# Optimization experiments

Hardware: AMD Instinct MI355X
Metric: run time of the kernel (lower is better)

## Reference

```python
import jax, jax.numpy as jnp
import numpy as np

B, N = 2, 1024
DIM, HEADS, DH, MLP = 768, 12, 64, 3072
PD = 768          # channels * patch_size^2 = 3*16*16
GRID = 16         # image_size // patch_size
DEPTH = 8
INNER = HEADS * DH


def layer_norm(x, g):
    # torch F.layer_norm with beta=0 buffer, eps=1e-5
    m = x.mean(-1, keepdims=True)
    v = ((x - m) ** 2).mean(-1, keepdims=True)
    return (x - m) / jnp.sqrt(v + 1e-5) * g


def qk_rmsnorm(x, g):
    # F.normalize(x, dim=-1) * sqrt(DH) * gamma ; gamma is [H,1,DH]
    n = jnp.linalg.norm(x, axis=-1, keepdims=True)
    return x / jnp.maximum(n, 1e-12) * (DH ** 0.5) * g


def setup_inputs() -> dict:
    key = jax.random.key(0)
    ks = jax.random.split(key, 16)
    s = 0.02
    d = {
        "patches": jax.random.normal(ks[0], (B, N, PD), dtype=jnp.float32),
        "h_idx": jax.random.randint(ks[1], (B, N), 0, GRID),
        "w_idx": jax.random.randint(ks[2], (B, N), 0, GRID),
        "image_ids": jnp.sort(jax.random.randint(ks[3], (B, N), 0, 8), axis=-1),
        "pos_h": jax.random.normal(ks[4], (GRID, PD)) * s,
        "pos_w": jax.random.normal(ks[5], (GRID, PD)) * s,
        "Wp": jax.random.normal(ks[6], (PD, DIM)) * s,
        "bp": jnp.zeros((DIM,)),
        "ln_p": jnp.ones((DIM,)),
        "ln1": jnp.ones((DEPTH, DIM)),
        "qg": jnp.ones((DEPTH, HEADS, 1, DH)),
        "kg": jnp.ones((DEPTH, HEADS, 1, DH)),
        "Wq": jax.random.normal(ks[7], (DEPTH, DIM, INNER)) * s,
        "Wkv": jax.random.normal(ks[8], (DEPTH, DIM, 2 * INNER)) * s,
        "Wo": jax.random.normal(ks[9], (DEPTH, INNER, DIM)) * s,
        "ln2": jnp.ones((DEPTH, DIM)),
        "W1": jax.random.normal(ks[10], (DEPTH, DIM, MLP)) * s,
        "b1": jnp.zeros((DEPTH, MLP)),
        "W2": jax.random.normal(ks[11], (DEPTH, MLP, DIM)) * s,
        "b2": jnp.zeros((DEPTH, DIM)),
        "lnf": jnp.ones((DIM,)),
    }
    return d


def reference(patches, h_idx, w_idx, image_ids, pos_h, pos_w, Wp, bp, ln_p,
              ln1, qg, kg, Wq, Wkv, Wo, ln2, W1, b1, W2, b2, lnf):
    # pos embed added to raw patches before projection (pos_embed_before_proj=True)
    x = patches + pos_h[h_idx] + pos_w[w_idx]            # [B,N,PD]
    x = layer_norm(x @ Wp + bp, ln_p)                    # [B,N,DIM]

    # block-diagonal attn_mask: tokens attend only within their own packed image
    mask = image_ids[:, None, :, None] == image_ids[:, None, None, :]  # [B,1,N,N]

    for i in range(DEPTH):
        xn = layer_norm(x, ln1[i])
        q = (xn @ Wq[i]).reshape(B, N, HEADS, DH).transpose(0, 2, 1, 3)
        k, v = jnp.split(xn @ Wkv[i], 2, axis=-1)
        k = k.reshape(B, N, HEADS, DH).transpose(0, 2, 1, 3)
        v = v.reshape(B, N, HEADS, DH).transpose(0, 2, 1, 3)
        q = qk_rmsnorm(q, qg[i])
        k = qk_rmsnorm(k, kg[i])
        dots = jnp.einsum('bhid,bhjd->bhij', q, k)       # [B,H,N,N]
        dots = jnp.where(mask, dots, -jnp.finfo(dots.dtype).max)
        attn = jax.nn.softmax(dots, axis=-1)
        o = jnp.einsum('bhij,bhjd->bhid', attn, v)
        o = o.transpose(0, 2, 1, 3).reshape(B, N, INNER)
        x = o @ Wo[i] + x
        h = jax.nn.gelu(layer_norm(x, ln2[i]) @ W1[i] + b1[i], approximate=False)
        x = (h @ W2[i] + b2[i]) + x
    return layer_norm(x, lnf)
```

## Files before the change

### kernel.cpp

```cpp
#include <hip/hip_runtime.h>
#include <hip/hip_bf16.h>
#include <math.h>

typedef _Float16 f16;
typedef f16   f16x8 __attribute__((ext_vector_type(8)));
typedef float f32x4 __attribute__((ext_vector_type(4)));
typedef unsigned short ushort_t;

#define DIM   768
#define HEADS 12
#define DH    64
#define MLP_  3072
#define NTOK  2048
#define SEQ   1024
#define WELTS 7077888

__device__ __forceinline__ ushort_t h2u(f16 h){ return __builtin_bit_cast(ushort_t, h); }
__device__ __forceinline__ unsigned pk2h(float a, float b){
  return (unsigned)h2u((f16)a) | ((unsigned)h2u((f16)b) << 16);
}
__device__ __forceinline__ void gload16(const void* g, void* l){
  __builtin_amdgcn_global_load_lds(
      (const __attribute__((address_space(1))) void*)g,
      (__attribute__((address_space(3))) void*)l, 16, 0, 0);
}
__device__ __forceinline__ float wred_sum(float v){
  #pragma unroll
  for (int o = 32; o > 0; o >>= 1) v += __shfl_xor(v, o);
  return v;
}

__global__ __launch_bounds__(256) void convert_w_kernel(
    const float* __restrict__ Wq, const float* __restrict__ Wkv,
    const float* __restrict__ Wo, const float* __restrict__ W1,
    const float* __restrict__ W2, int layer, int wp_only,
    f16* __restrict__ th)
{
  int bid = blockIdx.x;
  const float* src; int K, N; size_t ooff; int t;
  if (wp_only){ src = Wq; K = 768; N = 768; ooff = 0; t = bid; }
  else if (bid < 144) { src = Wq;  K = 768;  N = 768;  ooff = 0;       t = bid; }
  else if (bid < 432) { src = Wkv; K = 768;  N = 1536; ooff = 589824;  t = bid - 144; }
  else if (bid < 576) { src = Wo;  K = 768;  N = 768;  ooff = 1769472; t = bid - 432; }
  else if (bid < 1152){ src = W1;  K = 768;  N = 3072; ooff = 2359296; t = bid - 576; }
  else                { src = W2;  K = 3072; N = 768;  ooff = 4718592; t = bid - 1152; }
  if (!wp_only) src += (size_t)layer * K * N;
  int ntn = N >> 6;
  int tk = t / ntn, tn = t % ntn;
  int k0 = tk * 64, n0 = tn * 64;

  __shared__ unsigned lp[32][66];
  const int tid = threadIdx.x;
  #pragma unroll
  for (int p = 0; p < 2; p++){
    int rp = p * 16 + (tid >> 4);
    int c  = (tid & 15) * 4;
    const float* s0 = src + (size_t)(k0 + 2 * rp) * N + n0 + c;
    float4 a = *(const float4*)s0;
    float4 b = *(const float4*)(s0 + N);
    unsigned u0 = pk2h(a.x, b.x), u1 = pk2h(a.y, b.y);
    unsigned u2 = pk2h(a.z, b.z), u3 = pk2h(a.w, b.w);
    *(uint4*)&lp[rp][c] = make_uint4(u0, u1, u2, u3);
  }
  __syncthreads();
  #pragma unroll
  for (int p = 0; p < 2; p++){
    int n = p * 32 + (tid >> 3);
    int q = tid & 7;
    unsigned u[4];
    #pragma unroll
    for (int j = 0; j < 4; j++) u[j] = lp[q * 4 + j][n];
    *(uint4*)(th + ooff + (size_t)(n0 + n) * K + k0 + q * 8)
        = make_uint4(u[0], u[1], u[2], u[3]);
  }
}

__global__ __launch_bounds__(256) void gemm_big(
    const f16* __restrict__ Aq, const f16* __restrict__ Bw,
    const float* __restrict__ bias,
    f16* __restrict__ Cq,
    f16* __restrict__ Qh, f16* __restrict__ Kt, f16* __restrict__ Vt,
    const float* __restrict__ qgam, const float* __restrict__ kgam,
    int N, int K, int nbx, int mode)
{
  __shared__ __align__(16) f16 sA[128 * 64];
  __shared__ __align__(16) f16 sB[128 * 64];
  const int tid = threadIdx.x;
  const int wid = tid >> 6, lane = tid & 63;
  const int nwg = nbx << 4;
  const int bid = blockIdx.x;
  const int swz = (bid & 7) * (nwg >> 3) + (bid >> 3);
  const int by = swz & 15, bx = swz >> 4;
  const int brow = by << 7, bcol = bx << 7;
  const int m2 = wid & 1, n2 = wid >> 1;
  const int fr = lane & 15, fq = lane >> 4;
  const int Kc = K / (int)gridDim.z;
  const int kbase = (int)blockIdx.z * Kc;
  const int nk = Kc >> 6;

  const f16* pA = Aq + (size_t)brow * K + kbase;
  const f16* pB = Bw + (size_t)bcol * K + kbase;

  f32x4 acc[4][4] = {};

  for (int ks = 0; ks < nk; ks++){
    const int k0 = ks << 6;
    if (ks) __syncthreads();
    #pragma unroll
    for (int i = 0; i < 4; i++){
      int idx = tid + i * 256;
      int r = idx >> 3, c = idx & 7;
      int gc = c ^ (r & 7);
      gload16(pA + (size_t)r * K + k0 + gc * 8, &sA[idx * 8]);
      gload16(pB + (size_t)r * K + k0 + gc * 8, &sB[idx * 8]);
    }
    __syncthreads();
    #pragma unroll
    for (int s = 0; s < 2; s++){
      f16x8 a[4], b[4];
      #pragma unroll
      for (int m = 0; m < 4; m++){
        int r = m2 * 64 + m * 16 + fr;
        int ch = (s * 4 + fq) ^ (r & 7);
        a[m] = *(const f16x8*)(&sA[r * 64 + ch * 8]);
      }
      #pragma unroll
      for (int n = 0; n < 4; n++){
        int r = n2 * 64 + n * 16 + fr;
        int ch = (s * 4 + fq) ^ (r & 7);
        b[n] = *(const f16x8*)(&sB[r * 64 + ch * 8]);
      }
      #pragma unroll
      for (int m = 0; m < 4; m++)
        #pragma unroll
        for (int n = 0; n < 4; n++)
          acc[m][n] = __builtin_amdgcn_mfma_f32_16x16x32_f16(a[m], b[n], acc[m][n], 0, 0, 0);
    }
  }

  if (mode == 2){
    const int hbase = bcol + n2 * 64;
    if (hbase < 768){
      float gp[4];
      #pragma unroll
      for (int n = 0; n < 4; n++){
        int col = hbase + n * 16 + fr;
        gp[n] = qgam[col] * kgam[col];
      }
      #pragma unroll
      for (int m = 0; m < 4; m++)
        #pragma unroll
        for (int i = 0; i < 4; i++){
          float s = 0.f;
          #pragma unroll
          for (int n = 0; n < 4; n++) s += acc[m][n][i] * acc[m][n][i];
          s += __shfl_xor(s, 1); s += __shfl_xor(s, 2);
          s += __shfl_xor(s, 4); s += __shfl_xor(s, 8);
          float f = 8.f / fmaxf(sqrtf(s), 1e-12f);
          int row = brow + m2 * 64 + m * 16 + (fq << 2) + i;
          #pragma unroll
          for (int n = 0; n < 4; n++)
            Qh[(size_t)row * 768 + hbase + n * 16 + fr] = (f16)(acc[m][n][i] * f * gp[n]);
        }
    } else if (hbase < 1536){
      int hh = (hbase - 768) >> 6;
      #pragma unroll
      for (int m = 0; m < 4; m++)
        #pragma unroll
        for (int i = 0; i < 4; i++){
          float s = 0.f;
          #pragma unroll
          for (int n = 0; n < 4; n++) s += acc[m][n][i] * acc[m][n][i];
          s += __shfl_xor(s, 1); s += __shfl_xor(s, 2);
          s += __shfl_xor(s, 4); s += __shfl_xor(s, 8);
          float f = 8.f / fmaxf(sqrtf(s), 1e-12f);
          int row = brow + m2 * 64 + m * 16 + (fq << 2) + i;
          int bq = row >> 10, tok = row & 1023;
          #pragma unroll
          for (int n = 0; n < 4; n++)
            Kt[((size_t)(bq * 12 + hh) * 1024 + tok) * 64 + n * 16 + fr]
                = (f16)(acc[m][n][i] * f);
        }
    } else {
      int hh = (hbase - 1536) >> 6;
      #pragma unroll
      for (int n = 0; n < 4; n++){
        int dd = n * 16 + fr;
        #pragma unroll
        for (int m = 0; m < 4; m++){
          int row0 = brow + m2 * 64 + m * 16 + (fq << 2);
          int bq = row0 >> 10, tok0 = row0 & 1023;
          ushort4 sv;
          sv.x = h2u((f16)acc[m][n][0]); sv.y = h2u((f16)acc[m][n][1]);
          sv.z = h2u((f16)acc[m][n][2]); sv.w = h2u((f16)acc[m][n][3]);
          *(ushort4*)(Vt + ((size_t)((bq * 12 + hh) * 64 + dd)) * 1024 + tok0) = sv;
        }
      }
    }
  } else if (mode == 1){
    #pragma unroll
    for (int n = 0; n < 4; n++){
      int col = bcol + n2 * 64 + n * 16 + fr;
      float bv = bias[col];
      #pragma unroll
      for (int m = 0; m < 4; m++){
        int row0 = brow + m2 * 64 + m * 16 + (fq << 2);
        #pragma unroll
        for (int i = 0; i < 4; i++){
          float v = acc[m][n][i] + bv;
          float ge = 0.5f * v * (1.f + erff(v * 0.70710678118654752f));
          Cq[(size_t)(row0 + i) * N + col] = (f16)ge;
        }
      }
    }
  } else {
    f16* P = Cq + (size_t)blockIdx.z * ((size_t)NTOK * N);
    #pragma unroll
    for (int n = 0; n < 4; n++){
      int col = bcol + n2 * 64 + n * 16 + fr;
      #pragma unroll
      for (int m = 0; m < 4; m++){
        int row0 = brow + m2 * 64 + m * 16 + (fq << 2);
        #pragma unroll
        for (int i = 0; i < 4; i++)
          P[(size_t)(row0 + i) * N + col] = (f16)acc[m][n][i];
      }
    }
  }
}

__global__ __launch_bounds__(256) void gemm_small(
    const f16* __restrict__ Aq, const f16* __restrict__ Bw,
    const float* __restrict__ bias, const float* __restrict__ res,
    float* __restrict__ C, int N, int K, int nbx)
{
  __shared__ __align__(16) f16 sA[2][64 * 64];
  __shared__ __align__(16) f16 sB[2][64 * 64];
  const int tid = threadIdx.x;
  const int wid = tid >> 6, lane = tid & 63;
  const int nwg = nbx << 5;
  const int bid = blockIdx.x;
  const int swz = (bid & 7) * (nwg >> 3) + (bid >> 3);
  const int by = swz & 31, bx = swz >> 5;
  const int brow = by << 6, bcol = bx << 6;
  const int m2 = wid & 1, n2 = wid >> 1;
  const int fr = lane & 15, fq = lane >> 4;
  const int nk = K >> 6;

  const f16* pA = Aq + (size_t)brow * K;
  const f16* pB = Bw + (size_t)bcol * K;

  f32x4 acc[2][2] = {};

  auto STAGE = [&](int buf, int ks){
    const int k0 = ks << 6;
    #pragma unroll
    for (int i = 0; i < 2; i++){
      int idx = tid + i * 256;
      int r = idx >> 3, c = idx & 7;
      int gc = c ^ (r & 7);
      gload16(pA + (size_t)r * K + k0 + gc * 8, &sA[buf][idx * 8]);
      gload16(pB + (size_t)r * K + k0 + gc * 8, &sB[buf][idx * 8]);
    }
  };

  STAGE(0, 0);
  __syncthreads();
  int cur = 0;
  for (int ks = 0; ks < nk; ks++){
    if (ks + 1 < nk) STAGE(cur ^ 1, ks + 1);
    #pragma unroll
    for (int s = 0; s < 2; s++){
      f16x8 a[2], b[2];
      #pragma unroll
      for (int m = 0; m < 2; m++){
        int r = m2 * 32 + m * 16 + fr;
        int ch = (s * 4 + fq) ^ (r & 7);
        a[m] = *(const f16x8*)(&sA[cur][r * 64 + ch * 8]);
      }
      #pragma unroll
      for (int n = 0; n < 2; n++){
        int r = n2 * 32 + n * 16 + fr;
        int ch = (s * 4 + fq) ^ (r & 7);
        b[n] = *(const f16x8*)(&sB[cur][r * 64 + ch * 8]);
      }
      #pragma unroll
      for (int m = 0; m < 2; m++)
        #pragma unroll
        for (int n = 0; n < 2; n++)
          acc[m][n] = __builtin_amdgcn_mfma_f32_16x16x32_f16(a[m], b[n], acc[m][n], 0, 0, 0);
    }
    __syncthreads();
    cur ^= 1;
  }

  #pragma unroll
  for (int n = 0; n < 2; n++){
    int col = bcol + n2 * 32 + n * 16 + fr;
    float bv = bias ? bias[col] : 0.f;
    #pragma unroll
    for (int m = 0; m < 2; m++){
      int row0 = brow + m2 * 32 + m * 16 + (fq << 2);
      #pragma unroll
      for (int i = 0; i < 4; i++){
        float v = acc[m][n][i] + bv;
        size_t o = (size_t)(row0 + i) * N + col;
        if (res) v += res[o];
        C[o] = v;
      }
    }
  }
}

__global__ __launch_bounds__(256) void lnred_kernel(
    float* __restrict__ x, const f16* __restrict__ p, const float* __restrict__ badd,
    int npart, const float* __restrict__ g, f16* __restrict__ yq, float* __restrict__ yf)
{
  int wid = threadIdx.x >> 6, lane = threadIdx.x & 63;
  int row = blockIdx.x * 4 + wid;
  float* xr = x + (size_t)row * DIM;
  float v[12]; float s = 0.f;
  if (npart){
    #pragma unroll
    for (int d = 0; d < 12; d++){
      int c = d * 64 + lane;
      float t = xr[c] + badd[c];
      #pragma unroll
      for (int j = 0; j < 4; j++)
        t += (float)p[(size_t)j * (NTOK * DIM) + (size_t)row * DIM + c];
      xr[c] = t; v[d] = t; s += t;
    }
  } else {
    #pragma unroll
    for (int d = 0; d < 12; d++){ v[d] = xr[d * 64 + lane]; s += v[d]; }
  }
  s = wred_sum(s);
  float mean = s * (1.f / 768.f);
  float q2 = 0.f;
  #pragma unroll
  for (int d = 0; d < 12; d++){ float t = v[d] - mean; q2 += t * t; }
  q2 = wred_sum(q2);
  float rstd = rsqrtf(q2 * (1.f / 768.f) + 1e-5f);
  size_t base = (size_t)row * DIM;
  #pragma unroll
  for (int d = 0; d < 12; d++){
    float y = (v[d] - mean) * rstd * g[d * 64 + lane];
    if (yq) yq[base + d * 64 + lane] = (f16)y;
    else    yf[base + d * 64 + lane] = y;
  }
}

__global__ __launch_bounds__(256) void posadd_kernel(
    const float* __restrict__ patches, const int* __restrict__ hi,
    const int* __restrict__ wi, const float* __restrict__ ph,
    const float* __restrict__ pw, f16* __restrict__ oq)
{
  int idx = blockIdx.x * 256 + threadIdx.x;
  int tok = idx / 192, cv = idx % 192;
  float4 p = ((const float4*)patches)[idx];
  float4 a = *(const float4*)(ph + (size_t)hi[tok] * DIM + cv * 4);
  float4 b = *(const float4*)(pw + (size_t)wi[tok] * DIM + cv * 4);
  ushort4 o;
  o.x = h2u((f16)(p.x + a.x + b.x)); o.y = h2u((f16)(p.y + a.y + b.y));
  o.z = h2u((f16)(p.z + a.z + b.z)); o.w = h2u((f16)(p.w + a.w + b.w));
  ((ushort4*)oq)[idx] = o;
}

__global__ void seg_kernel(const int* __restrict__ ids, int2* __restrict__ segs)
{
  int i = blockIdx.x * 256 + threadIdx.x;
  int b = blockIdx.y;
  const int* row = ids + b * SEQ;
  int v = row[i];
  int lo = 0, hi = SEQ;
  while (lo < hi){ int mid = (lo + hi) >> 1; if (row[mid] <  v) lo = mid + 1; else hi = mid; }
  int s = lo;
  lo = 0; hi = SEQ;
  while (lo < hi){ int mid = (lo + hi) >> 1; if (row[mid] <= v) lo = mid + 1; else hi = mid; }
  segs[b * SEQ + i] = make_int2(s, lo);
}

__global__ __launch_bounds__(256) void attn_kernel(
    const f16* __restrict__ qh, const f16* __restrict__ ktp,
    const f16* __restrict__ vt, const int2* __restrict__ segs,
    f16* __restrict__ oq)
{
  __shared__ __align__(16) ushort_t Kq[32 * 64];
  __shared__ __align__(16) ushort_t Vl[64 * 40];

  const int tid = threadIdx.x;
  const int w = tid >> 6, lane = tid & 63;
  const int q15 = lane & 15, kg = lane >> 4;
  const int bh = blockIdx.x, b = bh / 12, h = bh % 12;
  const int qt = blockIdx.y;
  const int qrow = qt * 64 + w * 16 + q15;
  const size_t qtok = (size_t)b * SEQ + qrow;

  const f16* qp = qh + qtok * DIM + h * 64 + kg * 8;
  f16x8 qf[2];
  qf[0] = *(const f16x8*)(qp);
  qf[1] = *(const f16x8*)(qp + 32);

  const int2 se  = segs[qtok];
  const int2 se0 = segs[(size_t)b * SEQ + qt * 64];
  const int2 se1 = segs[(size_t)b * SEQ + qt * 64 + 63];
  const int klo = se0.x & ~31, khi = se1.y;

  float m = -3.0e38f, l = 0.f;
  f32x4 oacc[4] = {};

  const int krl = tid >> 3, kcl = tid & 7;
  const int kgc = kcl ^ (krl & 7);
  const f16* kbase = ktp + (size_t)bh * 1024 * 64;
  const int vd = tid >> 2, vko = (tid & 3) * 8;

  for (int kt0 = klo; kt0 < khi; kt0 += 32){
    gload16(kbase + (size_t)(kt0 + krl) * 64 + kgc * 8, Kq + tid * 8);
    {
      int ksrc = kt0 + vko;
      uint4 vv = *(const uint4*)(vt + ((size_t)bh * 64 + vd) * SEQ + ksrc);
      *(uint4*)((char*)Vl + vd * 80 + vko * 2) = vv;
    }
    __syncthreads();

    f32x4 s[2] = {};
    #pragma unroll
    for (int dh2 = 0; dh2 < 2; dh2++){
      #pragma unroll
      for (int khf = 0; khf < 2; khf++){
        int row = khf * 16 + q15;
        unsigned off = ((unsigned)row << 7) + ((unsigned)(dh2 * 4 + kg) << 4);
        off ^= (unsigned)(row & 7) << 4;
        f16x8 kf = *(const f16x8*)((const char*)Kq + off);
        s[khf] = __builtin_amdgcn_mfma_f32_16x16x32_f16(kf, qf[dh2], s[khf], 0, 0, 0);
      }
    }

    float p[8]; float tmax = -3.0e38f;
    #pragma unroll
    for (int khf = 0; khf < 2; khf++)
      #pragma unroll
      for (int i = 0; i < 4; i++){
        int key = kt0 + khf * 16 + kg * 4 + i;
        bool val = (key >= se.x) && (key < se.y);
        float sv = val ? s[khf][i] : -3.0e38f;
        p[khf * 4 + i] = sv;
        tmax = fmaxf(tmax, sv);
      }
    tmax = fmaxf(tmax, __shfl_xor(tmax, 16));
    tmax = fmaxf(tmax, __shfl_xor(tmax, 32));
    float mnew = fmaxf(m, tmax);
    float sc = __expf(m - mnew);
    float psum = 0.f;
    #pragma unroll
    for (int j = 0; j < 8; j++){
      float pv = (p[j] > -1.0e38f) ? __expf(p[j] - mnew) : 0.f;
      p[j] = pv; psum += pv;
    }
    psum += __shfl_xor(psum, 16);
    psum += __shfl_xor(psum, 32);
    l = l * sc + psum;
    m = mnew;
    #pragma unroll
    for (int dt = 0; dt < 4; dt++) oacc[dt] *= sc;

    unsigned u00 = pk2h(p[0], p[1]), u01 = pk2h(p[2], p[3]);
    unsigned u10 = pk2h(p[4], p[5]), u11 = pk2h(p[6], p[7]);
    int s0l = q15 + ((kg & 1) << 5);
    int s1l = s0l + 16;
    unsigned a0 = __shfl(u00, s0l), b0 = __shfl(u01, s0l);
    unsigned a1 = __shfl(u00, s1l), b1 = __shfl(u01, s1l);
    unsigned c0 = __shfl(u10, s0l), d0 = __shfl(u11, s0l);
    unsigned c1 = __shfl(u10, s1l), d1 = __shfl(u11, s1l);
    bool hih = kg >= 2;
    f16x8 pfrag = __builtin_bit_cast(f16x8,
        make_uint4(hih ? c0 : a0, hih ? d0 : b0, hih ? c1 : a1, hih ? d1 : b1));

    #pragma unroll
    for (int dt = 0; dt < 4; dt++){
      f16x8 vf = *(const f16x8*)((const char*)Vl + (dt * 16 + q15) * 80 + kg * 16);
      oacc[dt] = __builtin_amdgcn_mfma_f32_16x16x32_f16(vf, pfrag, oacc[dt], 0, 0, 0);
    }
    __syncthreads();
  }

  float rl = 1.f / l;
  size_t obase = qtok * DIM + h * 64;
  #pragma unroll
  for (int dt = 0; dt < 4; dt++){
    ushort4 hs;
    hs.x = h2u((f16)(oacc[dt][0] * rl)); hs.y = h2u((f16)(oacc[dt][1] * rl));
    hs.z = h2u((f16)(oacc[dt][2] * rl)); hs.w = h2u((f16)(oacc[dt][3] * rl));
    *(ushort4*)(oq + obase + dt * 16 + kg * 4) = hs;
  }
}

extern "C" void kernel_launch(void* const* d_in, const int* in_sizes, int n_in,
                              void* d_out, int out_size, void* d_ws, size_t ws_size,
                              hipStream_t stream)
{
  const float* patches   = (const float*)d_in[0];
  const int*   h_idx     = (const int*)d_in[1];
  const int*   w_idx     = (const int*)d_in[2];
  const int*   image_ids = (const int*)d_in[3];
  const float* pos_h = (const float*)d_in[4];
  const float* pos_w = (const float*)d_in[5];
  const float* Wp  = (const float*)d_in[6];
  const float* bp  = (const float*)d_in[7];
  const float* lnp = (const float*)d_in[8];
  const float* ln1 = (const float*)d_in[9];
  const float* qg  = (const float*)d_in[10];
  const float* kg  = (const float*)d_in[11];
  const float* Wq  = (const float*)d_in[12];
  const float* Wkv = (const float*)d_in[13];
  const float* Wo  = (const float*)d_in[14];
  const float* ln2 = (const float*)d_in[15];
  const float* W1  = (const float*)d_in[16];
  const float* b1  = (const float*)d_in[17];
  const float* W2  = (const float*)d_in[18];
  const float* b2  = (const float*)d_in[19];
  const float* lnf = (const float*)d_in[20];
  float* out = (float*)d_out;

  char* w = (char*)d_ws;
  float* x = (float*)w;            w += (size_t)NTOK * DIM * 4;
  f16* pbufh = (f16*)w;            w += (size_t)4 * NTOK * DIM * 2;
  f16* qh  = (f16*)w;              w += (size_t)NTOK * DIM * 2;
  f16* ktb = (f16*)w;              w += (size_t)NTOK * DIM * 2;
  f16* vtb = (f16*)w;              w += (size_t)NTOK * DIM * 2;
  f16* aAq = (f16*)w;              w += (size_t)NTOK * DIM * 2;
  f16* aBq = (f16*)w;              w += (size_t)NTOK * MLP_ * 2;
  int2* segs = (int2*)w;           w += (size_t)NTOK * 8;
  f16* wl = (f16*)w;
  float* ptmp = (float*)aBq;
  f16* wpc = pbufh;

  seg_kernel<<<dim3(4, 2), 256, 0, stream>>>(image_ids, segs);
  posadd_kernel<<<1536, 256, 0, stream>>>(patches, h_idx, w_idx, pos_h, pos_w, aAq);
  convert_w_kernel<<<144, 256, 0, stream>>>(Wp, nullptr, nullptr, nullptr, nullptr, 0, 1, wpc);
  gemm_small<<<384, 256, 0, stream>>>(aAq, wpc, bp, nullptr, ptmp, DIM, DIM, 12);
  lnred_kernel<<<NTOK / 4, 256, 0, stream>>>(ptmp, nullptr, nullptr, 0, lnp, nullptr, x);

  for (int i = 0; i < 8; i++){
    convert_w_kernel<<<1728, 256, 0, stream>>>(Wq, Wkv, Wo, W1, W2, i, 0, wl);
    lnred_kernel<<<NTOK / 4, 256, 0, stream>>>(
        x, pbufh, i ? (b2 + (i - 1) * DIM) : nullptr, i ? 4 : 0,
        ln1 + i * DIM, aAq, nullptr);
    gemm_big<<<288, 256, 0, stream>>>(
        aAq, wl, nullptr, nullptr, qh, ktb, vtb,
        qg + i * DIM, kg + i * DIM, 3 * DIM, DIM, 18, 2);
    attn_kernel<<<dim3(24, 16), 256, 0, stream>>>(qh, ktb, vtb, segs, aAq);
    gemm_small<<<384, 256, 0, stream>>>(
        aAq, wl + 1769472, nullptr, x, x, DIM, DIM, 12);
    lnred_kernel<<<NTOK / 4, 256, 0, stream>>>(
        x, nullptr, nullptr, 0, ln2 + i * DIM, aAq, nullptr);
    gemm_big<<<384, 256, 0, stream>>>(
        aAq, wl + 2359296, b1 + i * MLP_, aBq, nullptr, nullptr, nullptr,
        nullptr, nullptr, MLP_, DIM, 24, 1);
    gemm_big<<<dim3(96, 1, 4), 256, 0, stream>>>(
        aBq, wl + 4718592, nullptr, pbufh, nullptr, nullptr, nullptr,
        nullptr, nullptr, DIM, MLP_, 6, 3);
  }
  lnred_kernel<<<NTOK / 4, 256, 0, stream>>>(x, pbufh, b2 + 7 * DIM, 4, lnf, nullptr, out);
}
```

Baseline: 959.7 us.

## Overlap next-layer weight conversion with QKV GEMM and widen attention key tiles

Adds a fused launch in which the first 288 blocks run the QKV projection GEMM and the remaining blocks convert the next layer's fp32 weights to fp16 into a second buffer. This hides the per-layer conversion launch behind the QKV GEMM, and the weight workspace is double-buffered. The attention kernel now processes 64 keys per iteration instead of 32, with larger LDS tiles and two MFMAs per output tile, which halves the loop iterations and barriers. The trade-offs are more workspace, extra LDS in attention, and wasted key work at segment edges because tiles are now aligned to 64.

```diff
diff --git a/kernel.cpp b/kernel.cpp
--- a/kernel.cpp
+++ b/kernel.cpp
@@ -30,13 +30,12 @@
   return v;
 }
 
-__global__ __launch_bounds__(256) void convert_w_kernel(
-    const float* __restrict__ Wq, const float* __restrict__ Wkv,
+__device__ __forceinline__ void convert_body(
+    int bid, const float* __restrict__ Wq, const float* __restrict__ Wkv,
     const float* __restrict__ Wo, const float* __restrict__ W1,
     const float* __restrict__ W2, int layer, int wp_only,
     f16* __restrict__ th)
 {
-  int bid = blockIdx.x;
   const float* src; int K, N; size_t ooff; int t;
   if (wp_only){ src = Wq; K = 768; N = 768; ooff = 0; t = bid; }
   else if (bid < 144) { src = Wq;  K = 768;  N = 768;  ooff = 0;       t = bid; }
@@ -75,7 +74,17 @@
   }
 }
 
-__global__ __launch_bounds__(256) void gemm_big(
+__global__ __launch_bounds__(256) void convert_w_kernel(
+    const float* __restrict__ Wq, const float* __restrict__ Wkv,
+    const float* __restrict__ Wo, const float* __restrict__ W1,
+    const float* __restrict__ W2, int layer, int wp_only,
+    f16* __restrict__ th)
+{
+  convert_body(blockIdx.x, Wq, Wkv, Wo, W1, W2, layer, wp_only, th);
+}
+
+__device__ __forceinline__ void gemm_big_body(
+    int bid, int bz, int nz,
     const f16* __restrict__ Aq, const f16* __restrict__ Bw,
     const float* __restrict__ bias,
     f16* __restrict__ Cq,
@@ -88,14 +97,13 @@
   const int tid = threadIdx.x;
   const int wid = tid >> 6, lane = tid & 63;
   const int nwg = nbx << 4;
-  const int bid = blockIdx.x;
   const int swz = (bid & 7) * (nwg >> 3) + (bid >> 3);
   const int by = swz & 15, bx = swz >> 4;
   const int brow = by << 7, bcol = bx << 7;
   const int m2 = wid & 1, n2 = wid >> 1;
   const int fr = lane & 15, fq = lane >> 4;
-  const int Kc = K / (int)gridDim.z;
-  const int kbase = (int)blockIdx.z * Kc;
+  const int Kc = K / nz;
+  const int kbase = bz * Kc;
   const int nk = Kc >> 6;
 
   const f16* pA = Aq + (size_t)brow * K + kbase;
@@ -214,7 +222,7 @@
       }
     }
   } else {
-    f16* P = Cq + (size_t)blockIdx.z * ((size_t)NTOK * N);
+    f16* P = Cq + (size_t)bz * ((size_t)NTOK * N);
     #pragma unroll
     for (int n = 0; n < 4; n++){
       int col = bcol + n2 * 64 + n * 16 + fr;
@@ -227,6 +235,33 @@
       }
     }
   }
+}
+
+__global__ __launch_bounds__(256) void gemm_big(
+    const f16* __restrict__ Aq, const f16* __restrict__ Bw,
+    const float* __restrict__ bias,
+    f16* __restrict__ Cq,
+    f16* __restrict__ Qh, f16* __restrict__ Kt, f16* __restrict__ Vt,
+    const float* __restrict__ qgam, const float* __restrict__ kgam,
+    int N, int K, int nbx, int mode)
+{
+  gemm_big_body(blockIdx.x, blockIdx.z, (int)gridDim.z,
+                Aq, Bw, bias, Cq, Qh, Kt, Vt, qgam, kgam, N, K, nbx, mode);
+}
+
+__global__ __launch_bounds__(256) void qkvconv_kernel(
+    const f16* __restrict__ Aq, const f16* __restrict__ Bw,
+    f16* __restrict__ Qh, f16* __restrict__ Kt, f16* __restrict__ Vt,
+    const float* __restrict__ qgam, const float* __restrict__ kgam,
+    const float* __restrict__ Wq, const float* __restrict__ Wkv,
+    const float* __restrict__ Wo, const float* __restrict__ W1,
+    const float* __restrict__ W2, int nlayer, f16* __restrict__ thn)
+{
+  if (blockIdx.x < 288)
+    gemm_big_body((int)blockIdx.x, 0, 1, Aq, Bw, nullptr, nullptr,
+                  Qh, Kt, Vt, qgam, kgam, 3 * DIM, DIM, 18, 2);
+  else if (nlayer >= 0)
+    convert_body((int)blockIdx.x - 288, Wq, Wkv, Wo, W1, W2, nlayer, 0, thn);
 }
 
 __global__ __launch_bounds__(256) void gemm_small(
@@ -385,8 +420,8 @@
     const f16* __restrict__ vt, const int2* __restrict__ segs,
     f16* __restrict__ oq)
 {
-  __shared__ __align__(16) ushort_t Kq[32 * 64];
-  __shared__ __align__(16) ushort_t Vl[64 * 40];
+  __shared__ __align__(16) ushort_t Kq[64 * 64];
+  __shared__ __align__(16) ushort_t Vl[64 * 72];
 
   const int tid = threadIdx.x;
   const int w = tid >> 6, lane = tid & 63;
@@ -404,30 +439,35 @@
   const int2 se  = segs[qtok];
   const int2 se0 = segs[(size_t)b * SEQ + qt * 64];
   const int2 se1 = segs[(size_t)b * SEQ + qt * 64 + 63];
-  const int klo = se0.x & ~31, khi = se1.y;
+  const int klo = se0.x & ~63, khi = se1.y;
 
   float m = -3.0e38f, l = 0.f;
   f32x4 oacc[4] = {};
 
-  const int krl = tid >> 3, kcl = tid & 7;
-  const int kgc = kcl ^ (krl & 7);
   const f16* kbase = ktp + (size_t)bh * 1024 * 64;
-  const int vd = tid >> 2, vko = (tid & 3) * 8;
-
-  for (int kt0 = klo; kt0 < khi; kt0 += 32){
-    gload16(kbase + (size_t)(kt0 + krl) * 64 + kgc * 8, Kq + tid * 8);
-    {
-      int ksrc = kt0 + vko;
-      uint4 vv = *(const uint4*)(vt + ((size_t)bh * 64 + vd) * SEQ + ksrc);
-      *(uint4*)((char*)Vl + vd * 80 + vko * 2) = vv;
+  const int vd = tid >> 2, vc0 = tid & 3;
+
+  for (int kt0 = klo; kt0 < khi; kt0 += 64){
+    #pragma unroll
+    for (int i = 0; i < 2; i++){
+      int idx = tid + i * 256;
+      int r = idx >> 3, c = idx & 7;
+      int gc = c ^ (r & 7);
+      gload16(kbase + (size_t)(kt0 + r) * 64 + gc * 8, Kq + idx * 8);
+    }
+    #pragma unroll
+    for (int p2 = 0; p2 < 2; p2++){
+      int chunk = vc0 + p2 * 4;
+      uint4 vv = *(const uint4*)(vt + ((size_t)bh * 64 + vd) * SEQ + kt0 + chunk * 8);
+      *(uint4*)((char*)Vl + vd * 144 + chunk * 16) = vv;
     }
     __syncthreads();
 
-    f32x4 s[2] = {};
+    f32x4 s[4] = {};
     #pragma unroll
     for (int dh2 = 0; dh2 < 2; dh2++){
       #pragma unroll
-      for (int khf = 0; khf < 2; khf++){
+      for (int khf = 0; khf < 4; khf++){
         int row = khf * 16 + q15;
         unsigned off = ((unsigned)row << 7) + ((unsigned)(dh2 * 4 + kg) << 4);
         off ^= (unsigned)(row & 7) << 4;
@@ -436,9 +476,9 @@
       }
     }
 
-    float p[8]; float tmax = -3.0e38f;
-    #pragma unroll
-    for (int khf = 0; khf < 2; khf++)
+    float p[16]; float tmax = -3.0e38f;
+    #pragma unroll
+    for (int khf = 0; khf < 4; khf++)
       #pragma unroll
       for (int i = 0; i < 4; i++){
         int key = kt0 + khf * 16 + kg * 4 + i;
@@ -453,7 +493,7 @@
     float sc = __expf(m - mnew);
     float psum = 0.f;
     #pragma unroll
-    for (int j = 0; j < 8; j++){
+    for (int j = 0; j < 16; j++){
       float pv = (p[j] > -1.0e38f) ? __expf(p[j] - mnew) : 0.f;
       p[j] = pv; psum += pv;
     }
@@ -464,22 +504,33 @@
     #pragma unroll
     for (int dt = 0; dt < 4; dt++) oacc[dt] *= sc;
 
-    unsigned u00 = pk2h(p[0], p[1]), u01 = pk2h(p[2], p[3]);
-    unsigned u10 = pk2h(p[4], p[5]), u11 = pk2h(p[6], p[7]);
     int s0l = q15 + ((kg & 1) << 5);
     int s1l = s0l + 16;
-    unsigned a0 = __shfl(u00, s0l), b0 = __shfl(u01, s0l);
-    unsigned a1 = __shfl(u00, s1l), b1 = __shfl(u01, s1l);
-    unsigned c0 = __shfl(u10, s0l), d0 = __shfl(u11, s0l);
-    unsigned c1 = __shfl(u10, s1l), d1 = __shfl(u11, s1l);
     bool hih = kg >= 2;
-    f16x8 pfrag = __builtin_bit_cast(f16x8,
+    unsigned uA0 = pk2h(p[0],  p[1]),  uA1 = pk2h(p[2],  p[3]);
+    unsigned uA2 = pk2h(p[4],  p[5]),  uA3 = pk2h(p[6],  p[7]);
+    unsigned uB0 = pk2h(p[8],  p[9]),  uB1 = pk2h(p[10], p[11]);
+    unsigned uB2 = pk2h(p[12], p[13]), uB3 = pk2h(p[14], p[15]);
+    unsigned a0 = __shfl(uA0, s0l), b0 = __shfl(uA1, s0l);
+    unsigned a1 = __shfl(uA0, s1l), b1 = __shfl(uA1, s1l);
+    unsigned c0 = __shfl(uA2, s0l), d0 = __shfl(uA3, s0l);
+    unsigned c1 = __shfl(uA2, s1l), d1 = __shfl(uA3, s1l);
+    f16x8 pfA = __builtin_bit_cast(f16x8,
         make_uint4(hih ? c0 : a0, hih ? d0 : b0, hih ? c1 : a1, hih ? d1 : b1));
+    unsigned e0 = __shfl(uB0, s0l), f0 = __shfl(uB1, s0l);
+    unsigned e1 = __shfl(uB0, s1l), f1 = __shfl(uB1, s1l);
+    unsigned g0 = __shfl(uB2, s0l), h0 = __shfl(uB3, s0l);
+    unsigned g1 = __shfl(uB2, s1l), h1 = __shfl(uB3, s1l);
+    f16x8 pfB = __builtin_bit_cast(f16x8,
+        make_uint4(hih ? g0 : e0, hih ? h0 : f0, hih ? g1 : e1, hih ? h1 : f1));
 
     #pragma unroll
     for (int dt = 0; dt < 4; dt++){
-      f16x8 vf = *(const f16x8*)((const char*)Vl + (dt * 16 + q15) * 80 + kg * 16);
-      oacc[dt] = __builtin_amdgcn_mfma_f32_16x16x32_f16(vf, pfrag, oacc[dt], 0, 0, 0);
+      const char* vb = (const char*)Vl + (dt * 16 + q15) * 144 + kg * 16;
+      f16x8 vfA = *(const f16x8*)vb;
+      f16x8 vfB = *(const f16x8*)(vb + 64);
+      oacc[dt] = __builtin_amdgcn_mfma_f32_16x16x32_f16(vfA, pfA, oacc[dt], 0, 0, 0);
+      oacc[dt] = __builtin_amdgcn_mfma_f32_16x16x32_f16(vfB, pfB, oacc[dt], 0, 0, 0);
     }
     __syncthreads();
   }
@@ -531,7 +582,8 @@
   f16* aAq = (f16*)w;              w += (size_t)NTOK * DIM * 2;
   f16* aBq = (f16*)w;              w += (size_t)NTOK * MLP_ * 2;
   int2* segs = (int2*)w;           w += (size_t)NTOK * 8;
-  f16* wl = (f16*)w;
+  f16* wlA = (f16*)w;              w += (size_t)WELTS * 2;
+  f16* wlB = (f16*)w;
   float* ptmp = (float*)aBq;
   f16* wpc = pbufh;
 
@@ -540,25 +592,27 @@
   convert_w_kernel<<<144, 256, 0, stream>>>(Wp, nullptr, nullptr, nullptr, nullptr, 0, 1, wpc);
   gemm_small<<<384, 256, 0, stream>>>(aAq, wpc, bp, nullptr, ptmp, DIM, DIM, 12);
   lnred_kernel<<<NTOK / 4, 256, 0, stream>>>(ptmp, nullptr, nullptr, 0, lnp, nullptr, x);
+  convert_w_kernel<<<1728, 256, 0, stream>>>(Wq, Wkv, Wo, W1, W2, 0, 0, wlA);
 
   for (int i = 0; i < 8; i++){
-    convert_w_kernel<<<1728, 256, 0, stream>>>(Wq, Wkv, Wo, W1, W2, i, 0, wl);
+    f16* wcur = (i & 1) ? wlB : wlA;
+    f16* wnxt = (i & 1) ? wlA : wlB;
     lnred_kernel<<<NTOK / 4, 256, 0, stream>>>(
         x, pbufh, i ? (b2 + (i - 1) * DIM) : nullptr, i ? 4 : 0,
         ln1 + i * DIM, aAq, nullptr);
-    gemm_big<<<288, 256, 0, stream>>>(
-        aAq, wl, nullptr, nullptr, qh, ktb, vtb,
-        qg + i * DIM, kg + i * DIM, 3 * DIM, DIM, 18, 2);
+    qkvconv_kernel<<<2016, 256, 0, stream>>>(
+        aAq, wcur, qh, ktb, vtb, qg + i * DIM, kg + i * DIM,
+        Wq, Wkv, Wo, W1, W2, (i < 7) ? i + 1 : -1, wnxt);
     attn_kernel<<<dim3(24, 16), 256, 0, stream>>>(qh, ktb, vtb, segs, aAq);
     gemm_small<<<384, 256, 0, stream>>>(
-        aAq, wl + 1769472, nullptr, x, x, DIM, DIM, 12);
+        aAq, wcur + 1769472, nullptr, x, x, DIM, DIM, 12);
     lnred_kernel<<<NTOK / 4, 256, 0, stream>>>(
         x, nullptr, nullptr, 0, ln2 + i * DIM, aAq, nullptr);
     gemm_big<<<384, 256, 0, stream>>>(
-        aAq, wl + 2359296, b1 + i * MLP_, aBq, nullptr, nullptr, nullptr,
+        aAq, wcur + 2359296, b1 + i * MLP_, aBq, nullptr, nullptr, nullptr,
         nullptr, nullptr, MLP_, DIM, 24, 1);
     gemm_big<<<dim3(96, 1, 4), 256, 0, stream>>>(
-        aBq, wl + 4718592, nullptr, pbufh, nullptr, nullptr, nullptr,
+        aBq, wcur + 4718592, nullptr, pbufh, nullptr, nullptr, nullptr,
         nullptr, nullptr, DIM, MLP_, 6, 3);
   }
   lnred_kernel<<<NTOK / 4, 256, 0, stream>>>(x, pbufh, b2 + 7 * DIM, 4, lnf, nullptr, out);
```

Measured after the change: 906.7 us. 1.06x faster.
